# Optimization experiments

Measured on AMD Instinct MI355X. Metric: run time of the kernel, lower is better.

## Reference

```python
import jax, jax.numpy as jnp
import numpy as np

HEADS = 4
DIM_HEAD = 32
DIM = 128
HIDDEN = HEADS * DIM_HEAD  # 128
SCALE = DIM_HEAD ** -0.5


def setup_inputs() -> dict:
    key = jax.random.key(0)
    ks = jax.random.split(key, 7)
    b, c, h, w = 4, DIM, 256, 256
    x = jax.random.normal(ks[0], (b, c, h, w), dtype=jnp.float32)
    context = jax.random.normal(ks[1], (b, c, h, w), dtype=jnp.float32)
    # conv1x1 weights stored as [out, in] matrices
    s_in = 1.0 / np.sqrt(DIM)
    Wq = jax.random.uniform(ks[2], (HIDDEN, DIM), jnp.float32, -s_in, s_in)
    Wk = jax.random.uniform(ks[3], (HIDDEN, DIM), jnp.float32, -s_in, s_in)
    Wv = jax.random.uniform(ks[4], (HIDDEN, DIM), jnp.float32, -s_in, s_in)
    s_h = 1.0 / np.sqrt(HIDDEN)
    Wo = jax.random.uniform(ks[5], (DIM, HIDDEN), jnp.float32, -s_h, s_h)
    bo = jax.random.uniform(ks[6], (DIM,), jnp.float32, -s_h, s_h)
    return {"x": x, "context": context, "Wq": Wq, "Wk": Wk, "Wv": Wv, "Wo": Wo, "bo": bo}


def reference(x, context, Wq, Wk, Wv, Wo, bo):
    b, c, h, w = x.shape
    n = h * w
    xf = x.reshape(b, c, n)         # flatten spatial
    cf = context.reshape(b, c, n)
    # conv1x1 projections == channel matmuls
    q = jnp.einsum('oc,bcn->bon', Wq, xf).reshape(b, HEADS, DIM_HEAD, n)
    k = jnp.einsum('oc,bcn->bon', Wk, cf).reshape(b, HEADS, DIM_HEAD, n)
    v = jnp.einsum('oc,bcn->bon', Wv, cf).reshape(b, HEADS, DIM_HEAD, n)
    q = q * SCALE
    k = jax.nn.softmax(k, axis=-1)  # softmax over spatial positions
    ctx = jnp.einsum('bhdn,bhen->bhde', k, v)   # [b,h,d,e] small d_head x d_head
    out = jnp.einsum('bhde,bhdn->bhen', ctx, q)  # [b,h,e,n]
    out = out.reshape(b, HIDDEN, n)
    out = jnp.einsum('oc,bcn->bon', Wo, out) + bo[None, :, None]
    return out.reshape(b, c, h, w)
```

## Files before the change

kernel.cpp:

```cpp
#include <hip/hip_runtime.h>
#include <cstdint>
#include <cstddef>

typedef __bf16 bf16x8 __attribute__((ext_vector_type(8)));
typedef float f32x4 __attribute__((ext_vector_type(4)));
typedef unsigned int u32x4 __attribute__((ext_vector_type(4)));

#define MFMA16(a, b, c) __builtin_amdgcn_mfma_f32_16x16x32_bf16((a), (b), (c), 0, 0, 0)

static constexpr int CD = 128;
static constexpr int NTOK = 65536;
static constexpr float F_SCALE = 0.17677669529663688f;
static constexpr float F_LOG2E = 1.4426950408889634f;
static constexpr int K1_CB = 128;
static constexpr int PART = 4224;

__device__ __forceinline__ void gload_lds16(const float* g, void* l) {
  __builtin_amdgcn_global_load_lds(
      (const __attribute__((address_space(1))) void*)g,
      (__attribute__((address_space(3))) void*)l, 16, 0, 0);
}

__device__ __forceinline__ void stage_tile(const float* src_base, int n0,
                                           float* T1, int w, int lg, int l15) {
#pragma unroll
  for (int i = 0; i < 8; ++i) {
    int c = w * 32 + i * 4;
    const float* gp = src_base + (size_t)(c + lg) * NTOK + n0 + l15 * 4;
    gload_lds16(gp, (void*)(T1 + c * 64));
  }
}

__device__ __forceinline__ void transpose_tile(const float* T1, char* T2, int tid) {
  int nl = tid & 63;
  int xk = (nl & 7) << 4;
#pragma unroll
  for (int u = 0; u < 4; ++u) {
    int co = (tid >> 6) * 4 + u;
    u32x4 pk;
#pragma unroll
    for (int jj = 0; jj < 4; ++jj) {
      float f0 = T1[(co * 8 + 2 * jj) * 64 + nl];
      float f1 = T1[(co * 8 + 2 * jj + 1) * 64 + nl];
      unsigned short u0 = __builtin_bit_cast(unsigned short, (__bf16)f0);
      unsigned short u1 = __builtin_bit_cast(unsigned short, (__bf16)f1);
      pk[jj] = (unsigned int)u0 | ((unsigned int)u1 << 16);
    }
    *(u32x4*)(T2 + nl * 256 + ((co * 16) ^ xk)) = pk;
  }
}

__global__ __launch_bounds__(256, 2) void k1_ctx(
    const float* __restrict__ ctx_in, const float* __restrict__ Wk,
    const float* __restrict__ Wv, float* __restrict__ S_part) {
  __shared__ char smem[48 * 1024];
  float* T1 = (float*)smem;
  char* T2 = smem + 32 * 1024;
  char* EV = smem;

  const int tid = threadIdx.x;
  const int lane = tid & 63;
  const int w = tid >> 6;
  const int l15 = lane & 15;
  const int lg = lane >> 4;
  const int b = blockIdx.x >> 7;
  const int cb = blockIdx.x & 127;

  bf16x8 Af[4][4];
#pragma unroll
  for (int m = 0; m < 4; ++m) {
    const float* Wp = (m < 2) ? Wk : Wv;
    const float sc = (m < 2) ? F_LOG2E : 1.0f;
    int row = w * 32 + (m & 1) * 16 + l15;
#pragma unroll
    for (int s = 0; s < 4; ++s) {
      const float* p = Wp + row * CD + s * 32 + lg * 8;
#pragma unroll
      for (int e = 0; e < 8; ++e) Af[m][s][e] = (__bf16)(p[e] * sc);
    }
  }

  f32x4 Sacc[2][2];
#pragma unroll
  for (int i = 0; i < 2; ++i)
#pragma unroll
    for (int j = 0; j < 2; ++j) Sacc[i][j] = f32x4{0.f, 0.f, 0.f, 0.f};
  float zpart[2][4] = {{0.f, 0.f, 0.f, 0.f}, {0.f, 0.f, 0.f, 0.f}};

  const float* src_base = ctx_in + (size_t)b * CD * NTOK + cb * 512;
  const int xorr = (lane & 7) << 4;
  char* Ew = EV + w * 8192;
  char* Vw = EV + w * 8192 + 4096;

  for (int strip = 0; strip < 8; ++strip) {
    const int n0 = strip * 64;
    stage_tile(src_base, n0, T1, w, lg, l15);
    asm volatile("s_waitcnt vmcnt(0)" ::: "memory");
    __syncthreads();
    transpose_tile(T1, T2, tid);
    __syncthreads();

    f32x4 acc[4][4];
#pragma unroll
    for (int m = 0; m < 4; ++m)
#pragma unroll
      for (int t = 0; t < 4; ++t) acc[m][t] = f32x4{0.f, 0.f, 0.f, 0.f};
#pragma unroll
    for (int s = 0; s < 4; ++s) {
      bf16x8 Bf[4];
#pragma unroll
      for (int t = 0; t < 4; ++t) {
        int n = t * 16 + l15;
        Bf[t] = *(const bf16x8*)(T2 + n * 256 + ((s * 64 + lg * 16) ^ xorr));
      }
#pragma unroll
      for (int m = 0; m < 4; ++m)
#pragma unroll
        for (int t = 0; t < 4; ++t) acc[m][t] = MFMA16(Af[m][s], Bf[t], acc[m][t]);
    }

#pragma unroll
    for (int m = 0; m < 2; ++m)
#pragma unroll
      for (int t = 0; t < 4; ++t)
#pragma unroll
        for (int r = 0; r < 4; ++r) {
          float ev = __builtin_exp2f(acc[m][t][r]);
          zpart[m][r] += ev;
          int d = m * 16 + lg * 4 + r;
          int n = t * 16 + l15;
          *(__bf16*)(Ew + d * 128 + ((2 * n) ^ ((d & 7) << 4))) = (__bf16)ev;
          int e2 = d;
          *(__bf16*)(Vw + e2 * 128 + ((2 * n) ^ ((e2 & 7) << 4))) = (__bf16)acc[m + 2][t][r];
        }

#pragma unroll
    for (int s2 = 0; s2 < 2; ++s2) {
      bf16x8 Ea[2], Vb[2];
#pragma unroll
      for (int md = 0; md < 2; ++md) {
        int d = md * 16 + l15;
        Ea[md] = *(const bf16x8*)(Ew + d * 128 + ((s2 * 64 + lg * 16) ^ ((d & 7) << 4)));
        int e2 = md * 16 + l15;
        Vb[md] = *(const bf16x8*)(Vw + e2 * 128 + ((s2 * 64 + lg * 16) ^ ((e2 & 7) << 4)));
      }
#pragma unroll
      for (int md = 0; md < 2; ++md)
#pragma unroll
        for (int ne = 0; ne < 2; ++ne) Sacc[md][ne] = MFMA16(Ea[md], Vb[ne], Sacc[md][ne]);
    }
    __syncthreads();
  }

  float* outp = S_part + (size_t)(b * K1_CB + cb) * PART;
#pragma unroll
  for (int md = 0; md < 2; ++md)
#pragma unroll
    for (int ne = 0; ne < 2; ++ne)
#pragma unroll
      for (int r = 0; r < 4; ++r) {
        int d = md * 16 + lg * 4 + r;
        int e = ne * 16 + l15;
        outp[w * 1024 + d * 32 + e] = Sacc[md][ne][r];
      }
#pragma unroll
  for (int m = 0; m < 2; ++m)
#pragma unroll
    for (int r = 0; r < 4; ++r) {
      float z = zpart[m][r];
      z += __shfl_xor(z, 1, 16);
      z += __shfl_xor(z, 2, 16);
      z += __shfl_xor(z, 4, 16);
      z += __shfl_xor(z, 8, 16);
      if (l15 == 0) {
        int d = m * 16 + lg * 4 + r;
        outp[4096 + w * 32 + d] = z;
      }
    }
}

__global__ void k2a_reduce(const float* __restrict__ S_part, float* __restrict__ S_red,
                           float* __restrict__ Z_red) {
  int bid = blockIdx.x;
  int b = bid / 33, bs = bid % 33;
  int tid = threadIdx.x;
  __shared__ float red[256];
  int e_loc = tid & 127, half = tid >> 7;
  const float* base = S_part + (size_t)b * K1_CB * PART + (bs < 32 ? bs * 128 + e_loc : 4096 + e_loc);
  float sum = 0.f;
  for (int p = half * 64; p < half * 64 + 64; ++p) sum += base[(size_t)p * PART];
  red[tid] = sum;
  __syncthreads();
  if (tid < 128) {
    float v = red[tid] + red[tid + 128];
    if (bs < 32)
      S_red[b * 4096 + bs * 128 + tid] = v;
    else
      Z_red[b * 128 + tid] = v;
  }
}

__global__ void k2b_weff(const float* __restrict__ S_red, const float* __restrict__ Z_red,
                         const float* __restrict__ Wq, const float* __restrict__ Wo,
                         float* __restrict__ W_eff) {
  int b = blockIdx.x >> 3, og = blockIdx.x & 7;
  int tid = threadIdx.x;
  __shared__ float ctx_lds[4096];
  __shared__ float T_lds[16 * 128];
  for (int i = tid * 16; i < tid * 16 + 16; ++i)
    ctx_lds[i] = S_red[b * 4096 + i] / Z_red[b * 128 + (i >> 5)];
  __syncthreads();
  {
    int o_loc = tid >> 4, hd0 = (tid & 15) * 8;
    int o = og * 16 + o_loc;
    for (int j = 0; j < 8; ++j) {
      int hd = hd0 + j, h = hd >> 5, d = hd & 31;
      const float* wo = Wo + o * 128 + h * 32;
      const float* cx = ctx_lds + h * 1024 + d * 32;
      float acc = 0.f;
      for (int e = 0; e < 32; ++e) acc += wo[e] * cx[e];
      T_lds[o_loc * 128 + hd] = acc;
    }
  }
  __syncthreads();
  {
    int o_loc = tid >> 4, c0 = (tid & 15) * 8;
    float acc[8] = {};
    const float* Trow = T_lds + o_loc * 128;
    for (int hd = 0; hd < 128; ++hd) {
      float tv = Trow[hd];
      const float* wq = Wq + hd * 128 + c0;
#pragma unroll
      for (int j = 0; j < 8; ++j) acc[j] += tv * wq[j];
    }
    float* op = W_eff + b * 16384 + (og * 16 + o_loc) * 128 + c0;
#pragma unroll
    for (int j = 0; j < 8; ++j) op[j] = F_SCALE * acc[j];
  }
}

__global__ __launch_bounds__(256, 2) void k3_out(const float* __restrict__ x,
                                                 const float* __restrict__ W_eff,
                                                 const float* __restrict__ bo,
                                                 float* __restrict__ out) {
  __shared__ char smem[48 * 1024];
  float* T1 = (float*)smem;
  char* T2 = smem + 32 * 1024;
  const int tid = threadIdx.x;
  const int lane = tid & 63;
  const int w = tid >> 6;
  const int l15 = lane & 15;
  const int lg = lane >> 4;
  const int b = blockIdx.x >> 8;
  const int cb = blockIdx.x & 255;

  bf16x8 Af[2][4];
#pragma unroll
  for (int m = 0; m < 2; ++m) {
    int o = w * 32 + m * 16 + l15;
#pragma unroll
    for (int s = 0; s < 4; ++s) {
      const float* p = W_eff + b * 16384 + o * 128 + s * 32 + lg * 8;
#pragma unroll
      for (int e = 0; e < 8; ++e) Af[m][s][e] = (__bf16)p[e];
    }
  }
  float bof[2][4];
#pragma unroll
  for (int m = 0; m < 2; ++m)
#pragma unroll
    for (int r = 0; r < 4; ++r) bof[m][r] = bo[w * 32 + m * 16 + lg * 4 + r];

  const float* src_base = x + (size_t)b * CD * NTOK + cb * 256;
  float* out_base = out + (size_t)b * CD * NTOK + cb * 256;
  const int xorr = (lane & 7) << 4;

  for (int strip = 0; strip < 4; ++strip) {
    const int n0 = strip * 64;
    stage_tile(src_base, n0, T1, w, lg, l15);
    asm volatile("s_waitcnt vmcnt(0)" ::: "memory");
    __syncthreads();
    transpose_tile(T1, T2, tid);
    __syncthreads();

    f32x4 acc[2][4];
#pragma unroll
    for (int m = 0; m < 2; ++m)
#pragma unroll
      for (int t = 0; t < 4; ++t) acc[m][t] = f32x4{0.f, 0.f, 0.f, 0.f};
#pragma unroll
    for (int s = 0; s < 4; ++s) {
      bf16x8 Bf[4];
#pragma unroll
      for (int t = 0; t < 4; ++t) {
        int n = t * 16 + l15;
        Bf[t] = *(const bf16x8*)(T2 + n * 256 + ((s * 64 + lg * 16) ^ xorr));
      }
#pragma unroll
      for (int m = 0; m < 2; ++m)
#pragma unroll
        for (int t = 0; t < 4; ++t) acc[m][t] = MFMA16(Af[m][s], Bf[t], acc[m][t]);
    }
#pragma unroll
    for (int m = 0; m < 2; ++m)
#pragma unroll
      for (int t = 0; t < 4; ++t)
#pragma unroll
        for (int r = 0; r < 4; ++r) {
          int o = w * 32 + m * 16 + lg * 4 + r;
          out_base[(size_t)o * NTOK + n0 + t * 16 + l15] = acc[m][t][r] + bof[m][r];
        }
    __syncthreads();
  }
}

extern "C" void kernel_launch(void* const* d_in, const int* in_sizes, int n_in,
                              void* d_out, int out_size, void* d_ws, size_t ws_size,
                              hipStream_t stream) {
  const float* x = (const float*)d_in[0];
  const float* ctxg = (const float*)d_in[1];
  const float* Wq = (const float*)d_in[2];
  const float* Wk = (const float*)d_in[3];
  const float* Wv = (const float*)d_in[4];
  const float* Wo = (const float*)d_in[5];
  const float* bo = (const float*)d_in[6];
  float* out = (float*)d_out;

  float* ws = (float*)d_ws;
  float* S_part = ws;
  float* S_red = ws + 512 * PART;
  float* Z_red = S_red + 16384;
  float* W_eff = Z_red + 512;

  k1_ctx<<<dim3(512), dim3(256), 0, stream>>>(ctxg, Wk, Wv, S_part);
  k2a_reduce<<<dim3(132), dim3(256), 0, stream>>>(S_part, S_red, Z_red);
  k2b_weff<<<dim3(32), dim3(256), 0, stream>>>(S_red, Z_red, Wq, Wo, W_eff);
  k3_out<<<dim3(1024), dim3(256), 0, stream>>>(x, W_eff, bo, out);
}
```

Baseline: 174.6 us.

## Prefetch next strip, vectorize transpose and stores, swap MFMA operands, widen k1 grid

Both streaming kernels now issue the global-to-LDS load for the next 64-token strip before the current strip's MFMAs run. The old trailing barrier is dropped, and k1 gets separate LDS for the E/V scratch. The LDS transpose reads float4 from a swizzled staging layout. MFMA operand order is swapped so each lane holds contiguous tokens, which allows packed bf16 and float4 output stores and changes the S_part layout that k2b reads. k1 can also launch twice as many blocks with shorter strips when the workspace is large enough, and k3's launch bound is raised to 3 waves per SIMD. The cost is more LDS per k1 block (80KB), less occupancy there, and more register pressure.

```diff
diff --git a/kernel.cpp b/kernel.cpp
--- a/kernel.cpp
+++ b/kernel.cpp
@@ -5,6 +5,7 @@
 typedef __bf16 bf16x8 __attribute__((ext_vector_type(8)));
 typedef float f32x4 __attribute__((ext_vector_type(4)));
 typedef unsigned int u32x4 __attribute__((ext_vector_type(4)));
+typedef unsigned int u32x2 __attribute__((ext_vector_type(2)));
 
 #define MFMA16(a, b, c) __builtin_amdgcn_mfma_f32_16x16x32_bf16((a), (b), (c), 0, 0, 0)
 
@@ -12,7 +13,6 @@
 static constexpr int NTOK = 65536;
 static constexpr float F_SCALE = 0.17677669529663688f;
 static constexpr float F_LOG2E = 1.4426950408889634f;
-static constexpr int K1_CB = 128;
 static constexpr int PART = 4224;
 
 __device__ __forceinline__ void gload_lds16(const float* g, void* l) {
@@ -21,62 +21,71 @@
       (__attribute__((address_space(3))) void*)l, 16, 0, 0);
 }
 
-__device__ __forceinline__ void stage_tile(const float* src_base, int n0,
-                                           float* T1, int w, int lg, int l15) {
+__device__ __forceinline__ unsigned short bfb(float f) {
+  return __builtin_bit_cast(unsigned short, (__bf16)f);
+}
+__device__ __forceinline__ unsigned pk2(float a, float b) {
+  return (unsigned)bfb(a) | ((unsigned)bfb(b) << 16);
+}
+
+__device__ __forceinline__ void stage_swz(const float* src_base, float* T1,
+                                          int w, int lg, int l15) {
 #pragma unroll
   for (int i = 0; i < 8; ++i) {
-    int c = w * 32 + i * 4;
-    const float* gp = src_base + (size_t)(c + lg) * NTOK + n0 + l15 * 4;
-    gload_lds16(gp, (void*)(T1 + c * 64));
-  }
-}
-
-__device__ __forceinline__ void transpose_tile(const float* T1, char* T2, int tid) {
-  int nl = tid & 63;
-  int xk = (nl & 7) << 4;
-#pragma unroll
-  for (int u = 0; u < 4; ++u) {
-    int co = (tid >> 6) * 4 + u;
+    int c0 = w * 32 + i * 4;
+    int row = c0 + lg;
+    int g = l15 ^ ((row >> 3) & 3);
+    gload_lds16(src_base + (size_t)row * NTOK + g * 4, (void*)(T1 + c0 * 64));
+  }
+}
+
+__device__ __forceinline__ void transpose_vec(const float* T1, char* T2, int tid) {
+  const int co = tid >> 4;
+  const int nq = tid & 15;
+  const int lgl = co & 3;
+  f32x4 M[8];
+#pragma unroll
+  for (int i = 0; i < 8; ++i)
+    M[i] = *(const f32x4*)(T1 + (co * 8 + i) * 64 + ((nq ^ lgl) * 4));
+#pragma unroll
+  for (int j = 0; j < 4; ++j) {
+    int n = nq * 4 + j;
     u32x4 pk;
 #pragma unroll
-    for (int jj = 0; jj < 4; ++jj) {
-      float f0 = T1[(co * 8 + 2 * jj) * 64 + nl];
-      float f1 = T1[(co * 8 + 2 * jj + 1) * 64 + nl];
-      unsigned short u0 = __builtin_bit_cast(unsigned short, (__bf16)f0);
-      unsigned short u1 = __builtin_bit_cast(unsigned short, (__bf16)f1);
-      pk[jj] = (unsigned int)u0 | ((unsigned int)u1 << 16);
-    }
-    *(u32x4*)(T2 + nl * 256 + ((co * 16) ^ xk)) = pk;
+    for (int p = 0; p < 4; ++p)
+      pk[p] = pk2(M[2 * p][j], M[2 * p + 1][j]);
+    *(u32x4*)(T2 + n * 256 + ((co * 16) ^ ((n & 7) << 4))) = pk;
   }
 }
 
 __global__ __launch_bounds__(256, 2) void k1_ctx(
     const float* __restrict__ ctx_in, const float* __restrict__ Wk,
-    const float* __restrict__ Wv, float* __restrict__ S_part) {
-  __shared__ char smem[48 * 1024];
+    const float* __restrict__ Wv, float* __restrict__ S_part,
+    int cpb_log2, int nstrips) {
+  __shared__ char smem[80 * 1024];
   float* T1 = (float*)smem;
   char* T2 = smem + 32 * 1024;
-  char* EV = smem;
+  char* EV = smem + 48 * 1024;
 
   const int tid = threadIdx.x;
   const int lane = tid & 63;
   const int w = tid >> 6;
   const int l15 = lane & 15;
   const int lg = lane >> 4;
-  const int b = blockIdx.x >> 7;
-  const int cb = blockIdx.x & 127;
-
-  bf16x8 Af[4][4];
+  const int b = blockIdx.x >> cpb_log2;
+  const int cb = blockIdx.x & ((1 << cpb_log2) - 1);
+
+  bf16x8 Wf[4][4];
 #pragma unroll
   for (int m = 0; m < 4; ++m) {
     const float* Wp = (m < 2) ? Wk : Wv;
     const float sc = (m < 2) ? F_LOG2E : 1.0f;
     int row = w * 32 + (m & 1) * 16 + l15;
 #pragma unroll
-    for (int s = 0; s < 4; ++s) {
-      const float* p = Wp + row * CD + s * 32 + lg * 8;
-#pragma unroll
-      for (int e = 0; e < 8; ++e) Af[m][s][e] = (__bf16)(p[e] * sc);
+    for (int ks = 0; ks < 4; ++ks) {
+      const float* p = Wp + row * CD + ks * 32 + lg * 8;
+#pragma unroll
+      for (int e = 0; e < 8; ++e) Wf[m][ks][e] = (__bf16)(p[e] * sc);
     }
   }
 
@@ -85,20 +94,21 @@
   for (int i = 0; i < 2; ++i)
 #pragma unroll
     for (int j = 0; j < 2; ++j) Sacc[i][j] = f32x4{0.f, 0.f, 0.f, 0.f};
-  float zpart[2][4] = {{0.f, 0.f, 0.f, 0.f}, {0.f, 0.f, 0.f, 0.f}};
-
-  const float* src_base = ctx_in + (size_t)b * CD * NTOK + cb * 512;
-  const int xorr = (lane & 7) << 4;
+  float zacc[2] = {0.f, 0.f};
+
+  const float* src0 = ctx_in + (size_t)b * CD * NTOK + (size_t)cb * (nstrips * 64);
+  const int xorr = (l15 & 7) << 4;
   char* Ew = EV + w * 8192;
   char* Vw = EV + w * 8192 + 4096;
 
-  for (int strip = 0; strip < 8; ++strip) {
-    const int n0 = strip * 64;
-    stage_tile(src_base, n0, T1, w, lg, l15);
+  stage_swz(src0, T1, w, lg, l15);
+
+  for (int s = 0; s < nstrips; ++s) {
     asm volatile("s_waitcnt vmcnt(0)" ::: "memory");
     __syncthreads();
-    transpose_tile(T1, T2, tid);
+    transpose_vec(T1, T2, tid);
     __syncthreads();
+    if (s + 1 < nstrips) stage_swz(src0 + (s + 1) * 64, T1, w, lg, l15);
 
     f32x4 acc[4][4];
 #pragma unroll
@@ -106,33 +116,36 @@
 #pragma unroll
       for (int t = 0; t < 4; ++t) acc[m][t] = f32x4{0.f, 0.f, 0.f, 0.f};
 #pragma unroll
-    for (int s = 0; s < 4; ++s) {
-      bf16x8 Bf[4];
+    for (int ks = 0; ks < 4; ++ks) {
+      bf16x8 At[4];
 #pragma unroll
       for (int t = 0; t < 4; ++t) {
         int n = t * 16 + l15;
-        Bf[t] = *(const bf16x8*)(T2 + n * 256 + ((s * 64 + lg * 16) ^ xorr));
+        At[t] = *(const bf16x8*)(T2 + n * 256 + ((ks * 64 + lg * 16) ^ xorr));
       }
 #pragma unroll
       for (int m = 0; m < 4; ++m)
 #pragma unroll
-        for (int t = 0; t < 4; ++t) acc[m][t] = MFMA16(Af[m][s], Bf[t], acc[m][t]);
-    }
-
-#pragma unroll
-    for (int m = 0; m < 2; ++m)
-#pragma unroll
-      for (int t = 0; t < 4; ++t)
-#pragma unroll
-        for (int r = 0; r < 4; ++r) {
-          float ev = __builtin_exp2f(acc[m][t][r]);
-          zpart[m][r] += ev;
-          int d = m * 16 + lg * 4 + r;
-          int n = t * 16 + l15;
-          *(__bf16*)(Ew + d * 128 + ((2 * n) ^ ((d & 7) << 4))) = (__bf16)ev;
-          int e2 = d;
-          *(__bf16*)(Vw + e2 * 128 + ((2 * n) ^ ((e2 & 7) << 4))) = (__bf16)acc[m + 2][t][r];
-        }
+        for (int t = 0; t < 4; ++t) acc[m][t] = MFMA16(At[t], Wf[m][ks], acc[m][t]);
+    }
+
+#pragma unroll
+    for (int m = 0; m < 2; ++m) {
+      int d = m * 16 + l15;
+      int dx = (d & 7) << 4;
+#pragma unroll
+      for (int t = 0; t < 4; ++t) {
+        f32x4 a = acc[m][t];
+        float e0 = __builtin_exp2f(a[0]), e1 = __builtin_exp2f(a[1]);
+        float e2 = __builtin_exp2f(a[2]), e3 = __builtin_exp2f(a[3]);
+        zacc[m] += (e0 + e1) + (e2 + e3);
+        u32x2 pe{pk2(e0, e1), pk2(e2, e3)};
+        *(u32x2*)(Ew + d * 128 + ((t * 32 + lg * 8) ^ dx)) = pe;
+        f32x4 v = acc[m + 2][t];
+        u32x2 pv{pk2(v[0], v[1]), pk2(v[2], v[3])};
+        *(u32x2*)(Vw + d * 128 + ((t * 32 + lg * 8) ^ dx)) = pv;
+      }
+    }
 
 #pragma unroll
     for (int s2 = 0; s2 < 2; ++s2) {
@@ -140,55 +153,46 @@
 #pragma unroll
       for (int md = 0; md < 2; ++md) {
         int d = md * 16 + l15;
-        Ea[md] = *(const bf16x8*)(Ew + d * 128 + ((s2 * 64 + lg * 16) ^ ((d & 7) << 4)));
-        int e2 = md * 16 + l15;
-        Vb[md] = *(const bf16x8*)(Vw + e2 * 128 + ((s2 * 64 + lg * 16) ^ ((e2 & 7) << 4)));
+        int off = (s2 * 64 + lg * 16) ^ ((d & 7) << 4);
+        Ea[md] = *(const bf16x8*)(Ew + d * 128 + off);
+        Vb[md] = *(const bf16x8*)(Vw + d * 128 + off);
       }
 #pragma unroll
       for (int md = 0; md < 2; ++md)
 #pragma unroll
         for (int ne = 0; ne < 2; ++ne) Sacc[md][ne] = MFMA16(Ea[md], Vb[ne], Sacc[md][ne]);
     }
-    __syncthreads();
-  }
-
-  float* outp = S_part + (size_t)(b * K1_CB + cb) * PART;
+  }
+
+  float* outp = S_part + (size_t)blockIdx.x * PART;
 #pragma unroll
   for (int md = 0; md < 2; ++md)
 #pragma unroll
-    for (int ne = 0; ne < 2; ++ne)
-#pragma unroll
-      for (int r = 0; r < 4; ++r) {
-        int d = md * 16 + lg * 4 + r;
-        int e = ne * 16 + l15;
-        outp[w * 1024 + d * 32 + e] = Sacc[md][ne][r];
-      }
-#pragma unroll
-  for (int m = 0; m < 2; ++m)
-#pragma unroll
-    for (int r = 0; r < 4; ++r) {
-      float z = zpart[m][r];
-      z += __shfl_xor(z, 1, 16);
-      z += __shfl_xor(z, 2, 16);
-      z += __shfl_xor(z, 4, 16);
-      z += __shfl_xor(z, 8, 16);
-      if (l15 == 0) {
-        int d = m * 16 + lg * 4 + r;
-        outp[4096 + w * 32 + d] = z;
-      }
-    }
+    for (int ne = 0; ne < 2; ++ne) {
+      int e = ne * 16 + l15, d0 = md * 16 + lg * 4;
+      *(f32x4*)(outp + w * 1024 + e * 32 + d0) = Sacc[md][ne];
+    }
+#pragma unroll
+  for (int m = 0; m < 2; ++m) {
+    float z = zacc[m];
+    z += __shfl_xor(z, 16, 64);
+    z += __shfl_xor(z, 32, 64);
+    if (lg == 0) outp[4096 + w * 32 + m * 16 + l15] = z;
+  }
 }
 
 __global__ void k2a_reduce(const float* __restrict__ S_part, float* __restrict__ S_red,
-                           float* __restrict__ Z_red) {
+                           float* __restrict__ Z_red, int nparts) {
   int bid = blockIdx.x;
   int b = bid / 33, bs = bid % 33;
   int tid = threadIdx.x;
   __shared__ float red[256];
   int e_loc = tid & 127, half = tid >> 7;
-  const float* base = S_part + (size_t)b * K1_CB * PART + (bs < 32 ? bs * 128 + e_loc : 4096 + e_loc);
+  const float* base =
+      S_part + (size_t)b * nparts * PART + (bs < 32 ? bs * 128 + e_loc : 4096 + e_loc);
   float sum = 0.f;
-  for (int p = half * 64; p < half * 64 + 64; ++p) sum += base[(size_t)p * PART];
+  int h = nparts >> 1;
+  for (int p = half * h; p < half * h + h; ++p) sum += base[(size_t)p * PART];
   red[tid] = sum;
   __syncthreads();
   if (tid < 128) {
@@ -207,8 +211,10 @@
   int tid = threadIdx.x;
   __shared__ float ctx_lds[4096];
   __shared__ float T_lds[16 * 128];
-  for (int i = tid * 16; i < tid * 16 + 16; ++i)
-    ctx_lds[i] = S_red[b * 4096 + i] / Z_red[b * 128 + (i >> 5)];
+  for (int i = tid * 16; i < tid * 16 + 16; ++i) {
+    int hh = i >> 10, dd = i & 31;
+    ctx_lds[i] = S_red[b * 4096 + i] / Z_red[b * 128 + hh * 32 + dd];
+  }
   __syncthreads();
   {
     int o_loc = tid >> 4, hd0 = (tid & 15) * 8;
@@ -216,9 +222,9 @@
     for (int j = 0; j < 8; ++j) {
       int hd = hd0 + j, h = hd >> 5, d = hd & 31;
       const float* wo = Wo + o * 128 + h * 32;
-      const float* cx = ctx_lds + h * 1024 + d * 32;
+      const float* cx = ctx_lds + h * 1024 + d;
       float acc = 0.f;
-      for (int e = 0; e < 32; ++e) acc += wo[e] * cx[e];
+      for (int e = 0; e < 32; ++e) acc += wo[e] * cx[e * 32];
       T_lds[o_loc * 128 + hd] = acc;
     }
   }
@@ -239,7 +245,7 @@
   }
 }
 
-__global__ __launch_bounds__(256, 2) void k3_out(const float* __restrict__ x,
+__global__ __launch_bounds__(256, 3) void k3_out(const float* __restrict__ x,
                                                  const float* __restrict__ W_eff,
                                                  const float* __restrict__ bo,
                                                  float* __restrict__ out) {
@@ -254,34 +260,31 @@
   const int b = blockIdx.x >> 8;
   const int cb = blockIdx.x & 255;
 
-  bf16x8 Af[2][4];
+  bf16x8 Wf[2][4];
 #pragma unroll
   for (int m = 0; m < 2; ++m) {
     int o = w * 32 + m * 16 + l15;
 #pragma unroll
-    for (int s = 0; s < 4; ++s) {
-      const float* p = W_eff + b * 16384 + o * 128 + s * 32 + lg * 8;
-#pragma unroll
-      for (int e = 0; e < 8; ++e) Af[m][s][e] = (__bf16)p[e];
-    }
-  }
-  float bof[2][4];
-#pragma unroll
-  for (int m = 0; m < 2; ++m)
-#pragma unroll
-    for (int r = 0; r < 4; ++r) bof[m][r] = bo[w * 32 + m * 16 + lg * 4 + r];
-
-  const float* src_base = x + (size_t)b * CD * NTOK + cb * 256;
-  float* out_base = out + (size_t)b * CD * NTOK + cb * 256;
-  const int xorr = (lane & 7) << 4;
-
-  for (int strip = 0; strip < 4; ++strip) {
-    const int n0 = strip * 64;
-    stage_tile(src_base, n0, T1, w, lg, l15);
+    for (int ks = 0; ks < 4; ++ks) {
+      const float* p = W_eff + b * 16384 + o * 128 + ks * 32 + lg * 8;
+#pragma unroll
+      for (int e = 0; e < 8; ++e) Wf[m][ks][e] = (__bf16)p[e];
+    }
+  }
+  float bof[2] = {bo[w * 32 + l15], bo[w * 32 + 16 + l15]};
+
+  const float* src0 = x + (size_t)b * CD * NTOK + cb * 256;
+  float* out0 = out + (size_t)b * CD * NTOK + cb * 256;
+  const int xorr = (l15 & 7) << 4;
+
+  stage_swz(src0, T1, w, lg, l15);
+
+  for (int s = 0; s < 4; ++s) {
     asm volatile("s_waitcnt vmcnt(0)" ::: "memory");
     __syncthreads();
-    transpose_tile(T1, T2, tid);
+    transpose_vec(T1, T2, tid);
     __syncthreads();
+    if (s + 1 < 4) stage_swz(src0 + (s + 1) * 64, T1, w, lg, l15);
 
     f32x4 acc[2][4];
 #pragma unroll
@@ -289,28 +292,28 @@
 #pragma unroll
       for (int t = 0; t < 4; ++t) acc[m][t] = f32x4{0.f, 0.f, 0.f, 0.f};
 #pragma unroll
-    for (int s = 0; s < 4; ++s) {
-      bf16x8 Bf[4];
+    for (int ks = 0; ks < 4; ++ks) {
+      bf16x8 At[4];
 #pragma unroll
       for (int t = 0; t < 4; ++t) {
         int n = t * 16 + l15;
-        Bf[t] = *(const bf16x8*)(T2 + n * 256 + ((s * 64 + lg * 16) ^ xorr));
+        At[t] = *(const bf16x8*)(T2 + n * 256 + ((ks * 64 + lg * 16) ^ xorr));
       }
 #pragma unroll
       for (int m = 0; m < 2; ++m)
 #pragma unroll
-        for (int t = 0; t < 4; ++t) acc[m][t] = MFMA16(Af[m][s], Bf[t], acc[m][t]);
-    }
-#pragma unroll
-    for (int m = 0; m < 2; ++m)
-#pragma unroll
-      for (int t = 0; t < 4; ++t)
-#pragma unroll
-        for (int r = 0; r < 4; ++r) {
-          int o = w * 32 + m * 16 + lg * 4 + r;
-          out_base[(size_t)o * NTOK + n0 + t * 16 + l15] = acc[m][t][r] + bof[m][r];
-        }
-    __syncthreads();
+        for (int t = 0; t < 4; ++t) acc[m][t] = MFMA16(At[t], Wf[m][ks], acc[m][t]);
+    }
+#pragma unroll
+    for (int m = 0; m < 2; ++m) {
+      int o = w * 32 + m * 16 + l15;
+#pragma unroll
+      for (int t = 0; t < 4; ++t) {
+        f32x4 v = acc[m][t];
+        v[0] += bof[m]; v[1] += bof[m]; v[2] += bof[m]; v[3] += bof[m];
+        *(f32x4*)(out0 + (size_t)o * NTOK + s * 64 + t * 16 + lg * 4) = v;
+      }
+    }
   }
 }
 
@@ -326,14 +329,20 @@
   const float* bo = (const float*)d_in[6];
   float* out = (float*)d_out;
 
+  size_t need256 = ((size_t)1024 * PART + 16384 + 512 + 65536) * sizeof(float);
+  int cpb_log2, nstrips;
+  if (ws_size >= need256) { cpb_log2 = 8; nstrips = 4; }
+  else                    { cpb_log2 = 7; nstrips = 8; }
+  int nblk1 = 4 << cpb_log2;
+
   float* ws = (float*)d_ws;
   float* S_part = ws;
-  float* S_red = ws + 512 * PART;
+  float* S_red = ws + (size_t)nblk1 * PART;
   float* Z_red = S_red + 16384;
   float* W_eff = Z_red + 512;
 
-  k1_ctx<<<dim3(512), dim3(256), 0, stream>>>(ctxg, Wk, Wv, S_part);
-  k2a_reduce<<<dim3(132), dim3(256), 0, stream>>>(S_part, S_red, Z_red);
+  k1_ctx<<<dim3(nblk1), dim3(256), 0, stream>>>(ctxg, Wk, Wv, S_part, cpb_log2, nstrips);
+  k2a_reduce<<<dim3(132), dim3(256), 0, stream>>>(S_part, S_red, Z_red, 1 << cpb_log2);
   k2b_weff<<<dim3(32), dim3(256), 0, stream>>>(S_red, Z_red, Wq, Wo, W_eff);
   k3_out<<<dim3(1024), dim3(256), 0, stream>>>(x, W_eff, bo, out);
 }
```

Result: faster. 164.9 us (-5.5%).
